# Kernel optimization log

Measured on AMD Instinct MI355X. Metric: run time of the kernel, lower is better.

## Reference

```python
import jax, jax.numpy as jnp
import numpy as np
from jax import lax

TS = 1.0  # sampling time


def setup_inputs() -> dict:
    key = jax.random.key(0)
    k1, k2, k3, k4 = jax.random.split(key, 4)
    q, m, n_x, n_u, h = 8192, 2048, 2, 1, 64
    x0 = jax.random.normal(k1, (q, n_x), dtype=jnp.float32)
    u = jax.random.normal(k2, (m, q, n_u), dtype=jnp.float32)
    # small neural state-space model: f(x, u) = tanh([x, u] @ W1 + b1) @ W2 + b2
    W1 = jax.random.normal(k3, (n_x + n_u, h), dtype=jnp.float32) * (1.0 / np.sqrt(n_x + n_u))
    b1 = jnp.zeros((h,), dtype=jnp.float32)
    W2 = jax.random.normal(k4, (h, n_x), dtype=jnp.float32) * 0.01
    b2 = jnp.zeros((n_x,), dtype=jnp.float32)
    return {"x0": x0, "u": u, "W1": W1, "b1": b1, "W2": W2, "b2": b2}


def reference(x0, u, W1, b1, W2, b2):
    ts = TS
    dt2 = ts / 2.0

    def f(x, u_step):
        # x: (q, n_x), u_step: (q, n_u) -> dx: (q, n_x)
        h = jnp.tanh(jnp.concatenate([x, u_step], axis=-1) @ W1 + b1)
        return h @ W2 + b2

    def step(x, u_step):
        k1 = f(x, u_step)
        k2 = f(x + dt2 * k1, u_step)
        k3 = f(x + dt2 * k2, u_step)
        k4 = f(x + ts * k3, u_step)
        x_new = x + (ts / 6.0) * (k1 + 2.0 * k2 + 2.0 * k3 + k4)
        return x_new, x  # output is state BEFORE update (matches torch loop)

    _, X_sim = lax.scan(step, x0, u)
    return X_sim  # (m, q, n_x)
```

## Files before the change

### kernel.cpp

```cpp
#include <hip/hip_runtime.h>

#define QN 8192
#define MN 2048
#define HN 64
#define LPT 16
#define UPL 4

template <int CTRL>
__device__ __forceinline__ float dpp_add(float v) {
    int m = __builtin_amdgcn_update_dpp(0, __float_as_int(v), CTRL, 0xf, 0xf, true);
    return v + __int_as_float(m);
}
#define DPP_QUAD_XOR1 0xB1
#define DPP_QUAD_XOR2 0x4E
#define DPP_HALF_MIRR 0x141
#define DPP_ROW_MIRR  0x140

__global__ __launch_bounds__(256, 2) void rk4_nss_kernel(
    const float* __restrict__ x0p,
    const float* __restrict__ up,
    const float* __restrict__ W1,
    const float* __restrict__ b1,
    const float* __restrict__ W2,
    const float* __restrict__ b2,
    float* __restrict__ out)
{
    const int tid  = blockIdx.x * 256 + threadIdx.x;
    const int lane = threadIdx.x & (LPT - 1);
    const int traj = tid >> 4;
    if (traj >= QN) return;

    const float SC = 2.8853900817779268f;

    float ws10[UPL], ws11[UPL], ws12[UPL], bsb[UPL], w20n[UPL], w21n[UPL];
#pragma unroll
    for (int k = 0; k < UPL; ++k) {
        const int j = lane + k * LPT;
        ws10[k] = W1[j] * SC;
        ws11[k] = W1[HN + j] * SC;
        ws12[k] = W1[2 * HN + j] * SC;
        bsb[k]  = b1[j] * SC;
        w20n[k] = -2.0f * W2[2 * j];
        w21n[k] = -2.0f * W2[2 * j + 1];
    }
    float c0 = b2[0], c1 = b2[1];
    for (int j = 0; j < HN; ++j) {
        c0 += W2[2 * j];
        c1 += W2[2 * j + 1];
    }

    float xa = x0p[2 * traj];
    float xb = x0p[2 * traj + 1];
    float ucur = up[traj];

    float2* outv = reinterpret_cast<float2*>(out);

    float pb[UPL];

    auto feval = [&](float ia, float ib, float& d0, float& d1) {
        float dden[UPL];
#pragma unroll
        for (int k = 0; k < UPL; ++k) {
            float pre = fmaf(ws10[k], ia, fmaf(ws11[k], ib, pb[k]));
            pre = __builtin_amdgcn_fmed3f(pre, -43.0f, 43.0f);
            dden[k] = __builtin_amdgcn_exp2f(pre) + 1.0f;
        }
        float r01 = __builtin_amdgcn_rcpf(dden[0] * dden[1]);
        float r23 = __builtin_amdgcn_rcpf(dden[2] * dden[3]);
        float inv0 = r01 * dden[1];
        float inv1 = r01 * dden[0];
        float inv2 = r23 * dden[3];
        float inv3 = r23 * dden[2];

        float p0 = fmaf(inv0, w20n[0],
                   fmaf(inv1, w20n[1],
                   fmaf(inv2, w20n[2], inv3 * w20n[3])));
        float p1 = fmaf(inv0, w21n[0],
                   fmaf(inv1, w21n[1],
                   fmaf(inv2, w21n[2], inv3 * w21n[3])));

        p0 = dpp_add<DPP_QUAD_XOR1>(p0);  p1 = dpp_add<DPP_QUAD_XOR1>(p1);
        p0 = dpp_add<DPP_QUAD_XOR2>(p0);  p1 = dpp_add<DPP_QUAD_XOR2>(p1);
        p0 = dpp_add<DPP_HALF_MIRR>(p0);  p1 = dpp_add<DPP_HALF_MIRR>(p1);
        p0 = dpp_add<DPP_ROW_MIRR>(p0);   p1 = dpp_add<DPP_ROW_MIRR>(p1);
        d0 = p0 + c0;
        d1 = p1 + c1;
    };

    for (int t = 0; t < MN; ++t) {
        if (lane == 0) {
            outv[t * QN + traj] = make_float2(xa, xb);
        }
        const float unext = (t + 1 < MN) ? up[(t + 1) * QN + traj] : 0.0f;

#pragma unroll
        for (int k = 0; k < UPL; ++k)
            pb[k] = fmaf(ws12[k], ucur, bsb[k]);

        float k1a, k1b, k2a, k2b, k3a, k3b, k4a, k4b;
        feval(xa, xb, k1a, k1b);
        feval(fmaf(0.5f, k1a, xa), fmaf(0.5f, k1b, xb), k2a, k2b);
        feval(fmaf(0.5f, k2a, xa), fmaf(0.5f, k2b, xb), k3a, k3b);
        feval(xa + k3a, xb + k3b, k4a, k4b);

        float ta = k2a + k3a;
        float sa = k1a + k4a;
        xa = fmaf((1.0f / 6.0f), fmaf(2.0f, ta, sa), xa);
        float tb = k2b + k3b;
        float sb = k1b + k4b;
        xb = fmaf((1.0f / 6.0f), fmaf(2.0f, tb, sb), xb);
        ucur = unext;
    }
}

extern "C" void kernel_launch(void* const* d_in, const int* in_sizes, int n_in,
                              void* d_out, int out_size, void* d_ws, size_t ws_size,
                              hipStream_t stream) {
    const float* x0 = (const float*)d_in[0];
    const float* u  = (const float*)d_in[1];
    const float* W1 = (const float*)d_in[2];
    const float* b1 = (const float*)d_in[3];
    const float* W2 = (const float*)d_in[4];
    const float* b2 = (const float*)d_in[5];
    float* out = (float*)d_out;

    const int threads = 256;
    const int blocks  = (QN * LPT) / threads;
    rk4_nss_kernel<<<blocks, threads, 0, stream>>>(x0, u, W1, b1, W2, b2, out);
}
```

Measured before the change: 1.892 ms.

## Pack hidden-layer FMAs as float2, fold bias constant into RK stages, unroll by two

Hidden pre-activations are now computed with two-wide vector FMAs, which may map to packed FP32 instructions on CDNA. The b2 plus W2 column-sum constant is folded into precomputed half and full offsets of the state, so each function evaluation no longer adds it. The time loop is unrolled by two with input prefetch two steps ahead and a pointer-increment store, and the exp clamp bound is tightened. The DPP old operand is changed to the source value, and the early-exit guard is dropped, which is safe only because the grid exactly covers the trajectories. Regrouping the constant additions changes float rounding slightly.

```diff
diff --git a/kernel.cpp b/kernel.cpp
--- a/kernel.cpp
+++ b/kernel.cpp
@@ -1,4 +1,6 @@
 #include <hip/hip_runtime.h>
+
+typedef float v2f __attribute__((ext_vector_type(2)));
 
 #define QN 8192
 #define MN 2048
@@ -8,13 +10,18 @@
 
 template <int CTRL>
 __device__ __forceinline__ float dpp_add(float v) {
-    int m = __builtin_amdgcn_update_dpp(0, __float_as_int(v), CTRL, 0xf, 0xf, true);
+    int m = __builtin_amdgcn_update_dpp(__float_as_int(v), __float_as_int(v),
+                                        CTRL, 0xf, 0xf, true);
     return v + __int_as_float(m);
 }
 #define DPP_QUAD_XOR1 0xB1
 #define DPP_QUAD_XOR2 0x4E
 #define DPP_HALF_MIRR 0x141
 #define DPP_ROW_MIRR  0x140
+
+__device__ __forceinline__ v2f vfma(v2f a, v2f b, v2f c) {
+    return __builtin_elementwise_fma(a, b, c);
+}
 
 __global__ __launch_bounds__(256, 2) void rk4_nss_kernel(
     const float* __restrict__ x0p,
@@ -28,18 +35,19 @@
     const int tid  = blockIdx.x * 256 + threadIdx.x;
     const int lane = threadIdx.x & (LPT - 1);
     const int traj = tid >> 4;
-    if (traj >= QN) return;
 
     const float SC = 2.8853900817779268f;
+    const float CL = 27.0f;
 
-    float ws10[UPL], ws11[UPL], ws12[UPL], bsb[UPL], w20n[UPL], w21n[UPL];
+    v2f W10[2], W11[2], W12[2], BS[2];
+    float w20n[UPL], w21n[UPL];
 #pragma unroll
     for (int k = 0; k < UPL; ++k) {
         const int j = lane + k * LPT;
-        ws10[k] = W1[j] * SC;
-        ws11[k] = W1[HN + j] * SC;
-        ws12[k] = W1[2 * HN + j] * SC;
-        bsb[k]  = b1[j] * SC;
+        W10[k >> 1][k & 1] = W1[j] * SC;
+        W11[k >> 1][k & 1] = W1[HN + j] * SC;
+        W12[k >> 1][k & 1] = W1[2 * HN + j] * SC;
+        BS[k >> 1][k & 1]  = b1[j] * SC;
         w20n[k] = -2.0f * W2[2 * j];
         w21n[k] = -2.0f * W2[2 * j + 1];
     }
@@ -48,29 +56,33 @@
         c0 += W2[2 * j];
         c1 += W2[2 * j + 1];
     }
+    const float c0h = 0.5f * c0, c1h = 0.5f * c1;
 
     float xa = x0p[2 * traj];
     float xb = x0p[2 * traj + 1];
-    float ucur = up[traj];
 
-    float2* outv = reinterpret_cast<float2*>(out);
+    float2* op = reinterpret_cast<float2*>(out) + traj;
+    const bool writer = (lane == 0);
 
-    float pb[UPL];
+    v2f PB[2];
 
-    auto feval = [&](float ia, float ib, float& d0, float& d1) {
-        float dden[UPL];
-#pragma unroll
-        for (int k = 0; k < UPL; ++k) {
-            float pre = fmaf(ws10[k], ia, fmaf(ws11[k], ib, pb[k]));
-            pre = __builtin_amdgcn_fmed3f(pre, -43.0f, 43.0f);
-            dden[k] = __builtin_amdgcn_exp2f(pre) + 1.0f;
-        }
-        float r01 = __builtin_amdgcn_rcpf(dden[0] * dden[1]);
-        float r23 = __builtin_amdgcn_rcpf(dden[2] * dden[3]);
-        float inv0 = r01 * dden[1];
-        float inv1 = r01 * dden[0];
-        float inv2 = r23 * dden[3];
-        float inv3 = r23 * dden[2];
+    auto feval = [&](float ia, float ib, float& p0o, float& p1o) {
+        v2f IA = {ia, ia};
+        v2f IB = {ib, ib};
+        v2f PRE0 = vfma(W10[0], IA, vfma(W11[0], IB, PB[0]));
+        v2f PRE1 = vfma(W10[1], IA, vfma(W11[1], IB, PB[1]));
+        float den0 = __builtin_amdgcn_exp2f(__builtin_amdgcn_fmed3f(PRE0.x, -CL, CL)) + 1.0f;
+        float den1 = __builtin_amdgcn_exp2f(__builtin_amdgcn_fmed3f(PRE0.y, -CL, CL)) + 1.0f;
+        float den2 = __builtin_amdgcn_exp2f(__builtin_amdgcn_fmed3f(PRE1.x, -CL, CL)) + 1.0f;
+        float den3 = __builtin_amdgcn_exp2f(__builtin_amdgcn_fmed3f(PRE1.y, -CL, CL)) + 1.0f;
+        float d01 = den0 * den1;
+        float d23 = den2 * den3;
+        float r01 = __builtin_amdgcn_rcpf(d01);
+        float r23 = __builtin_amdgcn_rcpf(d23);
+        float inv0 = r01 * den1;
+        float inv1 = r01 * den0;
+        float inv2 = r23 * den3;
+        float inv3 = r23 * den2;
 
         float p0 = fmaf(inv0, w20n[0],
                    fmaf(inv1, w20n[1],
@@ -83,33 +95,47 @@
         p0 = dpp_add<DPP_QUAD_XOR2>(p0);  p1 = dpp_add<DPP_QUAD_XOR2>(p1);
         p0 = dpp_add<DPP_HALF_MIRR>(p0);  p1 = dpp_add<DPP_HALF_MIRR>(p1);
         p0 = dpp_add<DPP_ROW_MIRR>(p0);   p1 = dpp_add<DPP_ROW_MIRR>(p1);
-        d0 = p0 + c0;
-        d1 = p1 + c1;
+        p0o = p0;
+        p1o = p1;
     };
 
-    for (int t = 0; t < MN; ++t) {
-        if (lane == 0) {
-            outv[t * QN + traj] = make_float2(xa, xb);
-        }
-        const float unext = (t + 1 < MN) ? up[(t + 1) * QN + traj] : 0.0f;
+    auto step = [&](float u, int ) {
+        v2f UU = {u, u};
+        PB[0] = vfma(W12[0], UU, BS[0]);
+        PB[1] = vfma(W12[1], UU, BS[1]);
 
-#pragma unroll
-        for (int k = 0; k < UPL; ++k)
-            pb[k] = fmaf(ws12[k], ucur, bsb[k]);
+        const float xha = xa + c0h, xhb = xb + c1h;
+        const float xca = xa + c0,  xcb = xb + c1;
 
-        float k1a, k1b, k2a, k2b, k3a, k3b, k4a, k4b;
-        feval(xa, xb, k1a, k1b);
-        feval(fmaf(0.5f, k1a, xa), fmaf(0.5f, k1b, xb), k2a, k2b);
-        feval(fmaf(0.5f, k2a, xa), fmaf(0.5f, k2b, xb), k3a, k3b);
-        feval(xa + k3a, xb + k3b, k4a, k4b);
+        float p1a, p1b, p2a, p2b, p3a, p3b, p4a, p4b;
+        feval(xa, xb, p1a, p1b);
+        feval(fmaf(0.5f, p1a, xha), fmaf(0.5f, p1b, xhb), p2a, p2b);
+        feval(fmaf(0.5f, p2a, xha), fmaf(0.5f, p2b, xhb), p3a, p3b);
+        feval(xca + p3a, xcb + p3b, p4a, p4b);
 
-        float ta = k2a + k3a;
-        float sa = k1a + k4a;
-        xa = fmaf((1.0f / 6.0f), fmaf(2.0f, ta, sa), xa);
-        float tb = k2b + k3b;
-        float sb = k1b + k4b;
-        xb = fmaf((1.0f / 6.0f), fmaf(2.0f, tb, sb), xb);
-        ucur = unext;
+        float ta = p2a + p3a, sa = p1a + p4a;
+        xa = fmaf(1.0f / 6.0f, fmaf(2.0f, ta, sa), xca);
+        float tb = p2b + p3b, sb = p1b + p4b;
+        xb = fmaf(1.0f / 6.0f, fmaf(2.0f, tb, sb), xcb);
+    };
+
+    float u0 = up[traj];
+    float u1 = up[QN + traj];
+
+    for (int t = 0; t < MN; t += 2) {
+        const float u2 = (t + 2 < MN) ? up[(t + 2) * QN + traj] : 0.0f;
+        const float u3 = (t + 3 < MN) ? up[(t + 3) * QN + traj] : 0.0f;
+
+        if (writer) *op = make_float2(xa, xb);
+        op += QN;
+        step(u0, t);
+
+        if (writer) *op = make_float2(xa, xb);
+        op += QN;
+        step(u1, t + 1);
+
+        u0 = u2;
+        u1 = u3;
     }
 }
 
```

Result: faster. 1.826 ms (-3.5%).
